# Performance work log

Hardware: AMD Instinct MI355X
Metric: run time of the kernel (lower is better)

## Reference

```python
import jax, jax.numpy as jnp
import numpy as np

B, S, D = 1, 2048, 2048      # batch, seq, hidden
E, F, K = 64, 512, 8         # experts, expert ffn dim, top_k


def setup_inputs() -> dict:
    key = jax.random.key(0)
    ks = jax.random.split(key, 7)
    hidden_states = jax.random.normal(ks[0], (B, S, D), jnp.float32)
    gate_w = jax.random.normal(ks[1], (E, D), jnp.float32) * (D ** -0.5)   # router Linear weight
    w_gate = jax.random.normal(ks[2], (E, F, D), jnp.float32) * 0.02       # expert gate_proj
    w_up   = jax.random.normal(ks[3], (E, F, D), jnp.float32) * 0.02       # expert up_proj
    w_down = jax.random.normal(ks[4], (E, D, F), jnp.float32) * 0.02       # expert down_proj
    token_mod  = jax.random.randint(ks[5], (B * S,), -1, 2).astype(jnp.int32)  # {-1,0,1}
    expert_mod = jax.random.randint(ks[6], (E,), -1, 2).astype(jnp.int32)      # {-1,0,1}
    return {"hidden_states": hidden_states, "gate_w": gate_w, "w_gate": w_gate,
            "w_up": w_up, "w_down": w_down, "token_mod": token_mod,
            "expert_mod": expert_mod}


def reference(hidden_states, gate_w, w_gate, w_up, w_down, token_mod, expert_mod):
    bs = B * S
    x = hidden_states.reshape(bs, D)
    # router gate (Linear, no bias): [bs, E]
    logits = x @ gate_w.T
    # modality pre-filtering: mismatch (tok*exp == -1) -> -inf before softmax
    mismatch = (token_mod[:, None] * expert_mod[None, :]) == -1
    logits = jnp.where(mismatch, -jnp.inf, logits)
    probs = jax.nn.softmax(logits, axis=-1)
    rw, sel = jax.lax.top_k(probs, K)                       # [bs,K]
    rw = rw / jnp.sum(rw, axis=-1, keepdims=True)           # renormalize
    # scatter into sparse routing tensor [bs, E]
    sparse = jnp.zeros((bs, E), x.dtype).at[jnp.arange(bs)[:, None], sel].set(rw)
    # expert dispatch (SwiGLU experts), weighted-sum combine
    g = jnp.einsum('td,efd->tef', x, w_gate)                # [bs,E,F]
    u = jnp.einsum('td,efd->tef', x, w_up)
    h = jax.nn.silu(g) * u
    out = jnp.einsum('te,tef,edf->td', sparse, h, w_down)   # [bs,D]
    return out.reshape(B, S, D)
```

## Files before the change

### kernel.cpp

```cpp
#include <hip/hip_runtime.h>
#include <math.h>

#define BS   2048
#define DIM  2048
#define NE   64
#define NF   512
#define TOPK 8
#define MAXT 320

typedef __attribute__((ext_vector_type(8))) short bf16x8;
typedef __attribute__((ext_vector_type(4))) float f32x4;

__device__ __forceinline__ unsigned cvt2(float lo, float hi) {
    unsigned r;
    asm("v_cvt_pk_bf16_f32 %0, %1, %2" : "=v"(r) : "v"(lo), "v"(hi));
    return r;
}
__device__ __forceinline__ unsigned short f2bf(float f) {
    return (unsigned short)(cvt2(f, 0.f) & 0xFFFF);
}

#define SWZ(r, b) (((((r) << 7) + (b)) ^ (((r) & 7) << 4)))

__global__ __launch_bounds__(256) void zero_kernel(float* __restrict__ out, int* __restrict__ count)
{
    const size_t idx = (size_t)blockIdx.x * blockDim.x + threadIdx.x;
    const size_t tot = (size_t)BS * DIM;
    for (size_t i = idx * 4; i < tot; i += (size_t)gridDim.x * blockDim.x * 4) {
        *(float4*)&out[i] = make_float4(0.f, 0.f, 0.f, 0.f);
    }
    if (idx < NE) count[idx] = 0;
}

__global__ __launch_bounds__(256) void cvt_x_kernel(const float* __restrict__ x,
                                                    unsigned short* __restrict__ xb)
{
    const int idx = blockIdx.x * 256 + threadIdx.x;
    const int tot = BS * DIM / 4;
    for (int i = idx; i < tot; i += gridDim.x * 256) {
        const float4 v = *(const float4*)&x[i * 4];
        *(uint2*)&xb[i * 4] = make_uint2(cvt2(v.x, v.y), cvt2(v.z, v.w));
    }
}

__global__ __launch_bounds__(256) void router_kernel(
    const float* __restrict__ x, const float* __restrict__ gate_w,
    const int* __restrict__ token_mod, const int* __restrict__ expert_mod,
    int* __restrict__ count, int* __restrict__ list_token, float* __restrict__ list_w)
{
    __shared__ float xs[4 * DIM];
    __shared__ float pr[4][NE];
    const int t0  = blockIdx.x * 4;
    const int tid = threadIdx.x;
    const int lane = tid & 63, wave = tid >> 6;

    float4* xs4 = (float4*)xs;
    const float4* xr = (const float4*)(x + (size_t)t0 * DIM);
    for (int i = tid; i < 4 * (DIM / 4); i += 256) xs4[i] = xr[i];
    __syncthreads();

    for (int j = 0; j < 16; ++j) {
        const int e = wave * 16 + j;
        const float4* gw = (const float4*)(gate_w + (size_t)e * DIM);
        float s0 = 0.f, s1 = 0.f, s2 = 0.f, s3 = 0.f;
        for (int i = lane; i < DIM / 4; i += 64) {
            const float4 g  = gw[i];
            const float4 v0 = xs4[0 * 512 + i];
            const float4 v1 = xs4[1 * 512 + i];
            const float4 v2 = xs4[2 * 512 + i];
            const float4 v3 = xs4[3 * 512 + i];
            s0 += v0.x * g.x + v0.y * g.y + v0.z * g.z + v0.w * g.w;
            s1 += v1.x * g.x + v1.y * g.y + v1.z * g.z + v1.w * g.w;
            s2 += v2.x * g.x + v2.y * g.y + v2.z * g.z + v2.w * g.w;
            s3 += v3.x * g.x + v3.y * g.y + v3.z * g.z + v3.w * g.w;
        }
        #pragma unroll
        for (int off = 32; off > 0; off >>= 1) {
            s0 += __shfl_xor(s0, off, 64);
            s1 += __shfl_xor(s1, off, 64);
            s2 += __shfl_xor(s2, off, 64);
            s3 += __shfl_xor(s3, off, 64);
        }
        if (lane == 0) {
            pr[0][e] = s0; pr[1][e] = s1; pr[2][e] = s2; pr[3][e] = s3;
        }
    }
    __syncthreads();

    {
        const int t  = t0 + wave;
        const int tm = token_mod[t];
        const int em = expert_mod[lane];
        float p = pr[wave][lane];
        if (tm * em == -1) p = -INFINITY;
        float m0 = p;
        #pragma unroll
        for (int off = 32; off > 0; off >>= 1) m0 = fmaxf(m0, __shfl_xor(m0, off, 64));
        p = __expf(p - m0);
        float s8 = 0.f, wsel = 0.f;
        int   esel = 0;
        #pragma unroll
        for (int k = 0; k < TOPK; ++k) {
            float m = p;
            #pragma unroll
            for (int off = 32; off > 0; off >>= 1) m = fmaxf(m, __shfl_xor(m, off, 64));
            const unsigned long long b = __ballot(p == m);
            const int bi = __ffsll((unsigned long long)b) - 1;
            if (lane == bi) p = -1.f;
            if (lane == k) { esel = bi; wsel = m; }
            s8 += m;
        }
        const float inv = 1.f / s8;
        if (lane < TOPK) {
            const int pos = atomicAdd(&count[esel], 1);
            list_token[esel * BS + pos] = t;
            list_w[esel * BS + pos]     = wsel * inv;
        }
    }
}

__global__ void scan_kernel(const int* __restrict__ count, int* __restrict__ offsets,
                            int* __restrict__ worklist, int* __restrict__ ntiles)
{
    if (threadIdx.x == 0) {
        int s = 0, nt = 0;
        for (int e = 0; e < NE; ++e) {
            offsets[e] = s;
            for (int m0 = 0; m0 < count[e]; m0 += 64) worklist[nt++] = (e << 16) | m0;
            s += count[e];
        }
        ntiles[0] = nt;
    }
}

#define GU_X   0
#define GU_G   8192
#define GU_U   16384

#define GU_COMPUTE()                                                                  \
    {                                                                                 \
        _Pragma("unroll")                                                             \
        for (int ks = 0; ks < 2; ++ks) {                                              \
            const int kb = (ks * 32 + (lane >> 4) * 8) * 2;                           \
            bf16x8 a[2], bg[2], bu[2];                                                \
            _Pragma("unroll")                                                         \
            for (int m = 0; m < 2; ++m)                                               \
                a[m] = *(const bf16x8*)&lds[GU_X + SWZ(wr * 32 + m * 16 + (lane & 15), kb)]; \
            _Pragma("unroll")                                                         \
            for (int nn = 0; nn < 2; ++nn) {                                          \
                const int r = wc * 32 + nn * 16 + (lane & 15);                        \
                bg[nn] = *(const bf16x8*)&lds[GU_G + SWZ(r, kb)];                     \
                bu[nn] = *(const bf16x8*)&lds[GU_U + SWZ(r, kb)];                     \
            }                                                                         \
            _Pragma("unroll")                                                         \
            for (int m = 0; m < 2; ++m)                                               \
                _Pragma("unroll")                                                     \
                for (int nn = 0; nn < 2; ++nn) {                                      \
                    accg[m][nn] = __builtin_amdgcn_mfma_f32_16x16x32_bf16(a[m], bg[nn], accg[m][nn], 0, 0, 0); \
                    accu[m][nn] = __builtin_amdgcn_mfma_f32_16x16x32_bf16(a[m], bu[nn], accu[m][nn], 0, 0, 0); \
                }                                                                     \
        }                                                                             \
    }

#define GU_WRITE()                                                                    \
    {                                                                                 \
        _Pragma("unroll")                                                             \
        for (int i = 0; i < 2; ++i)                                                   \
            *(uint4*)&lds[GU_X + SWZ(xr0 + i * 32, xb0 * 16)] = lxx[i];               \
        _Pragma("unroll")                                                             \
        for (int i = 0; i < 4; ++i) {                                                 \
            const int r = rr + i * 16;                                                \
            *(uint2*)&lds[GU_G + SWZ(r, c4 * 8)] = make_uint2(cvt2(lg[i].x, lg[i].y), cvt2(lg[i].z, lg[i].w)); \
            *(uint2*)&lds[GU_U + SWZ(r, c4 * 8)] = make_uint2(cvt2(lu[i].x, lu[i].y), cvt2(lu[i].z, lu[i].w)); \
        }                                                                             \
    }

__global__ __launch_bounds__(256, 3) void gateup_mfma(
    const unsigned short* __restrict__ xb,
    const float* __restrict__ w_gate, const float* __restrict__ w_up,
    const int* __restrict__ count, const int* __restrict__ offsets,
    const int* __restrict__ worklist, const int* __restrict__ ntiles,
    const int* __restrict__ list_token, const float* __restrict__ list_w,
    unsigned short* __restrict__ h)
{
    if ((int)blockIdx.y >= ntiles[0]) return;
    const int wl = worklist[blockIdx.y];
    const int e  = wl >> 16;
    const int m0 = wl & 0xFFFF;
    const int f0 = blockIdx.x * 64;
    const int mc = min(64, count[e] - m0);

    __shared__ char  lds[24576];
    __shared__ int   toks[64];
    __shared__ float rws[64];

    const int tid = threadIdx.x;
    if (tid < 64) {
        const int idx = e * BS + m0 + (tid < mc ? tid : 0);
        toks[tid] = list_token[idx];
        rws[tid]  = (tid < mc) ? list_w[idx] : 0.f;
    }
    __syncthreads();

    const int lane = tid & 63, wave = tid >> 6;
    const int wr = wave >> 1, wc = wave & 1;
    const int rr = tid >> 4;
    const int c4 = tid & 15;
    const int xr0 = tid >> 3;
    const int xb0 = tid & 7;

    const unsigned short* xrow[2];
    #pragma unroll
    for (int i = 0; i < 2; ++i)
        xrow[i] = xb + (size_t)toks[xr0 + i * 32] * DIM + xb0 * 8;
    const float* grow[4];
    const float* urow[4];
    #pragma unroll
    for (int i = 0; i < 4; ++i) {
        grow[i] = w_gate + (size_t)e * NF * DIM + (size_t)(f0 + rr + i * 16) * DIM + c4 * 4;
        urow[i] = w_up   + (size_t)e * NF * DIM + (size_t)(f0 + rr + i * 16) * DIM + c4 * 4;
    }

    f32x4 accg[2][2] = {};
    f32x4 accu[2][2] = {};
    uint4  lxx[2];
    float4 lg[4], lu[4];

    #pragma unroll
    for (int i = 0; i < 2; ++i) lxx[i] = *(const uint4*)(xrow[i]);
    #pragma unroll
    for (int i = 0; i < 4; ++i) {
        lg[i] = *(const float4*)(grow[i]);
        lu[i] = *(const float4*)(urow[i]);
    }
    GU_WRITE();
    __syncthreads();

    for (int t = 0; t < DIM / 64 - 1; ++t) {
        const int doff = (t + 1) * 64;
        #pragma unroll
        for (int i = 0; i < 2; ++i) lxx[i] = *(const uint4*)(xrow[i] + doff);
        #pragma unroll
        for (int i = 0; i < 4; ++i) {
            lg[i] = *(const float4*)(grow[i] + doff);
            lu[i] = *(const float4*)(urow[i] + doff);
        }
        __builtin_amdgcn_sched_barrier(0);
        GU_COMPUTE();
        __syncthreads();
        GU_WRITE();
        __syncthreads();
    }
    GU_COMPUTE();

    const int base = offsets[e] + m0;
    #pragma unroll
    for (int m = 0; m < 2; ++m) {
        #pragma unroll
        for (int j = 0; j < 4; ++j) {
            const int tl = wr * 32 + m * 16 + (lane >> 4) * 4 + j;
            if (tl < mc) {
                const float w = rws[tl];
                #pragma unroll
                for (int nn = 0; nn < 2; ++nn) {
                    const int fl = f0 + wc * 32 + nn * 16 + (lane & 15);
                    const float g  = accg[m][nn][j];
                    const float u  = accu[m][nn][j];
                    const float hv = w * u * (g / (1.f + __expf(-g)));
                    h[(size_t)(base + tl) * NF + fl] = f2bf(hv);
                }
            }
        }
    }
}

#define DK_H   0
#define DK_W   8192

#define DK_COMPUTE()                                                                  \
    {                                                                                 \
        _Pragma("unroll")                                                             \
        for (int ks = 0; ks < 2; ++ks) {                                              \
            const int kb = (ks * 32 + (lane >> 4) * 8) * 2;                           \
            bf16x8 a[2], b[4];                                                        \
            _Pragma("unroll")                                                         \
            for (int m = 0; m < 2; ++m)                                               \
                a[m] = *(const bf16x8*)&lds[DK_H + SWZ(wr * 32 + m * 16 + (lane & 15), kb)]; \
            _Pragma("unroll")                                                         \
            for (int nn = 0; nn < 4; ++nn)                                            \
                b[nn] = *(const bf16x8*)&lds[DK_W + SWZ(wc * 64 + nn * 16 + (lane & 15), kb)]; \
            _Pragma("unroll")                                                         \
            for (int m = 0; m < 2; ++m)                                               \
                _Pragma("unroll")                                                     \
                for (int nn = 0; nn < 4; ++nn)                                        \
                    acc[m][nn] = __builtin_amdgcn_mfma_f32_16x16x32_bf16(a[m], b[nn], acc[m][nn], 0, 0, 0); \
        }                                                                             \
    }

#define DK_WRITE()                                                                    \
    {                                                                                 \
        _Pragma("unroll")                                                             \
        for (int i = 0; i < 2; ++i)                                                   \
            *(uint4*)&lds[DK_H + SWZ(hr + i * 32, hc * 2)] = lh[i];                   \
        _Pragma("unroll")                                                             \
        for (int i = 0; i < 8; ++i)                                                   \
            *(uint2*)&lds[DK_W + SWZ(rr + i * 16, c4 * 8)] = make_uint2(cvt2(lw[i].x, lw[i].y), cvt2(lw[i].z, lw[i].w)); \
    }

__global__ __launch_bounds__(256, 3) void down_mfma(
    const float* __restrict__ w_down,
    const int* __restrict__ count, const int* __restrict__ offsets,
    const int* __restrict__ worklist, const int* __restrict__ ntiles,
    const int* __restrict__ list_token,
    const unsigned short* __restrict__ h, float* __restrict__ out)
{
    if ((int)blockIdx.y >= ntiles[0]) return;
    const int wl = worklist[blockIdx.y];
    const int e  = wl >> 16;
    const int m0 = wl & 0xFFFF;
    const int d0 = blockIdx.x * 128;
    const int mc = min(64, count[e] - m0);

    __shared__ char lds[24576];
    __shared__ int  toks[64];

    const int tid = threadIdx.x;
    if (tid < 64) toks[tid] = list_token[e * BS + m0 + (tid < mc ? tid : 0)];
    __syncthreads();

    const int lane = tid & 63, wave = tid >> 6;
    const int wr = wave >> 1, wc = wave & 1;
    const int rr = tid >> 4;
    const int c4 = tid & 15;
    const int hr = tid >> 3;
    const int hc = (tid & 7) * 8;

    const float* wd  = w_down + (size_t)e * DIM * NF;
    const int   base = offsets[e] + m0;

    const unsigned short* hrow[2];
    #pragma unroll
    for (int i = 0; i < 2; ++i) {
        const int r  = hr + i * 32;
        const int rs = (r < mc ? r : 0);
        hrow[i] = h + (size_t)(base + rs) * NF + hc;
    }
    const float* wrow[8];
    #pragma unroll
    for (int i = 0; i < 8; ++i) wrow[i] = wd + (size_t)(d0 + rr + i * 16) * NF + c4 * 4;

    f32x4 acc[2][4] = {};
    uint4  lh[2];
    float4 lw[8];

    #pragma unroll
    for (int i = 0; i < 2; ++i) lh[i] = *(const uint4*)(hrow[i]);
    #pragma unroll
    for (int i = 0; i < 8; ++i) lw[i] = *(const float4*)(wrow[i]);
    DK_WRITE();
    __syncthreads();

    for (int t = 0; t < NF / 64 - 1; ++t) {
        const int foff = (t + 1) * 64;
        #pragma unroll
        for (int i = 0; i < 2; ++i) lh[i] = *(const uint4*)(hrow[i] + foff);
        #pragma unroll
        for (int i = 0; i < 8; ++i) lw[i] = *(const float4*)(wrow[i] + foff);
        __builtin_amdgcn_sched_barrier(0);
        DK_COMPUTE();
        __syncthreads();
        DK_WRITE();
        __syncthreads();
    }
    DK_COMPUTE();

    #pragma unroll
    for (int m = 0; m < 2; ++m)
        #pragma unroll
        for (int j = 0; j < 4; ++j) {
            const int sl = wr * 32 + m * 16 + (lane >> 4) * 4 + j;
            if (sl < mc) {
                float* orow = out + (size_t)toks[sl] * DIM + d0 + wc * 64 + (lane & 15);
                #pragma unroll
                for (int nn = 0; nn < 4; ++nn)
                    atomicAdd(&orow[nn * 16], acc[m][nn][j]);
            }
        }
}

extern "C" void kernel_launch(void* const* d_in, const int* in_sizes, int n_in,
                              void* d_out, int out_size, void* d_ws, size_t ws_size,
                              hipStream_t stream)
{
    const float* x          = (const float*)d_in[0];
    const float* gate_w     = (const float*)d_in[1];
    const float* w_gate     = (const float*)d_in[2];
    const float* w_up       = (const float*)d_in[3];
    const float* w_down     = (const float*)d_in[4];
    const int*   token_mod  = (const int*)d_in[5];
    const int*   expert_mod = (const int*)d_in[6];
    float* out = (float*)d_out;

    char* ws = (char*)d_ws;
    unsigned short* h  = (unsigned short*)ws;
    unsigned short* xb = (unsigned short*)(ws + 16777216);
    int*   count      = (int*)(ws + 25165824);
    int*   offsets    = (int*)(ws + 25166080);
    int*   ntiles     = (int*)(ws + 25166336);
    int*   worklist   = (int*)(ws + 25166592);
    int*   list_token = (int*)(ws + 25168640);
    float* list_w     = (float*)(ws + 25692928);

    zero_kernel<<<2048, 256, 0, stream>>>(out, count);
    cvt_x_kernel<<<1024, 256, 0, stream>>>(x, xb);
    router_kernel<<<BS / 4, 256, 0, stream>>>(x, gate_w, token_mod, expert_mod,
                                              count, list_token, list_w);
    scan_kernel<<<1, 64, 0, stream>>>(count, offsets, worklist, ntiles);

    dim3 g1(NF / 64, MAXT);
    gateup_mfma<<<g1, 256, 0, stream>>>(xb, w_gate, w_up, count, offsets,
                                        worklist, ntiles, list_token, list_w, h);
    dim3 g2(DIM / 128, MAXT);
    down_mfma<<<g2, 256, 0, stream>>>(w_down, count, offsets, worklist, ntiles,
                                      list_token, h, out);
}
```

Before: 625.9 us.

## Drop LDS staging; load MFMA operands directly from global with register double-buffering

Both expert GEMM kernels stop staging x/h and weight tiles through shared memory. Each lane now loads its MFMA fragments straight from global memory, converting weights to bf16 in registers, and double-buffers the loads across k-steps with no barriers. This removes the LDS round trip and the __syncthreads pairs. The cost is that weight rows are no longer shared between the waves in a block, so there are more global loads and more register pressure, and the occupancy bound is lowered from 3 to 2.

```diff
diff --git a/kernel.cpp b/kernel.cpp
--- a/kernel.cpp
+++ b/kernel.cpp
@@ -19,8 +19,12 @@
 __device__ __forceinline__ unsigned short f2bf(float f) {
     return (unsigned short)(cvt2(f, 0.f) & 0xFFFF);
 }
-
-#define SWZ(r, b) (((((r) << 7) + (b)) ^ (((r) & 7) << 4)))
+__device__ __forceinline__ bf16x8 pk8(float4 lo, float4 hi) {
+    union { bf16x8 v; unsigned u[4]; } r;
+    r.u[0] = cvt2(lo.x, lo.y); r.u[1] = cvt2(lo.z, lo.w);
+    r.u[2] = cvt2(hi.x, hi.y); r.u[3] = cvt2(hi.z, hi.w);
+    return r.v;
+}
 
 __global__ __launch_bounds__(256) void zero_kernel(float* __restrict__ out, int* __restrict__ count)
 {
@@ -133,49 +137,40 @@
     }
 }
 
-#define GU_X   0
-#define GU_G   8192
-#define GU_U   16384
-
-#define GU_COMPUTE()                                                                  \
-    {                                                                                 \
-        _Pragma("unroll")                                                             \
-        for (int ks = 0; ks < 2; ++ks) {                                              \
-            const int kb = (ks * 32 + (lane >> 4) * 8) * 2;                           \
-            bf16x8 a[2], bg[2], bu[2];                                                \
-            _Pragma("unroll")                                                         \
-            for (int m = 0; m < 2; ++m)                                               \
-                a[m] = *(const bf16x8*)&lds[GU_X + SWZ(wr * 32 + m * 16 + (lane & 15), kb)]; \
-            _Pragma("unroll")                                                         \
-            for (int nn = 0; nn < 2; ++nn) {                                          \
-                const int r = wc * 32 + nn * 16 + (lane & 15);                        \
-                bg[nn] = *(const bf16x8*)&lds[GU_G + SWZ(r, kb)];                     \
-                bu[nn] = *(const bf16x8*)&lds[GU_U + SWZ(r, kb)];                     \
-            }                                                                         \
-            _Pragma("unroll")                                                         \
-            for (int m = 0; m < 2; ++m)                                               \
-                _Pragma("unroll")                                                     \
-                for (int nn = 0; nn < 2; ++nn) {                                      \
-                    accg[m][nn] = __builtin_amdgcn_mfma_f32_16x16x32_bf16(a[m], bg[nn], accg[m][nn], 0, 0, 0); \
-                    accu[m][nn] = __builtin_amdgcn_mfma_f32_16x16x32_bf16(a[m], bu[nn], accu[m][nn], 0, 0, 0); \
-                }                                                                     \
-        }                                                                             \
-    }
-
-#define GU_WRITE()                                                                    \
-    {                                                                                 \
-        _Pragma("unroll")                                                             \
-        for (int i = 0; i < 2; ++i)                                                   \
-            *(uint4*)&lds[GU_X + SWZ(xr0 + i * 32, xb0 * 16)] = lxx[i];               \
-        _Pragma("unroll")                                                             \
-        for (int i = 0; i < 4; ++i) {                                                 \
-            const int r = rr + i * 16;                                                \
-            *(uint2*)&lds[GU_G + SWZ(r, c4 * 8)] = make_uint2(cvt2(lg[i].x, lg[i].y), cvt2(lg[i].z, lg[i].w)); \
-            *(uint2*)&lds[GU_U + SWZ(r, c4 * 8)] = make_uint2(cvt2(lu[i].x, lu[i].y), cvt2(lu[i].z, lu[i].w)); \
-        }                                                                             \
-    }
-
-__global__ __launch_bounds__(256, 3) void gateup_mfma(
+struct B8 { float4 v[8]; };
+
+
+#define GU_LOADB(BUF, KO)                                                     \
+    {                                                                         \
+        _Pragma("unroll")                                                     \
+        for (int nn = 0; nn < 2; ++nn) {                                      \
+            (BUF).v[nn * 2 + 0] = *(const float4*)(gp[nn] + (KO));            \
+            (BUF).v[nn * 2 + 1] = *(const float4*)(gp[nn] + (KO) + 4);        \
+            (BUF).v[4 + nn * 2 + 0] = *(const float4*)(up[nn] + (KO));        \
+            (BUF).v[4 + nn * 2 + 1] = *(const float4*)(up[nn] + (KO) + 4);    \
+        }                                                                     \
+    }
+
+#define GU_STEP(BUF, KO)                                                      \
+    {                                                                         \
+        bf16x8 a[2], bg[2], bu[2];                                            \
+        _Pragma("unroll")                                                     \
+        for (int m = 0; m < 2; ++m) a[m] = *(const bf16x8*)(aptr[m] + (KO));  \
+        _Pragma("unroll")                                                     \
+        for (int nn = 0; nn < 2; ++nn) {                                      \
+            bg[nn] = pk8((BUF).v[nn * 2], (BUF).v[nn * 2 + 1]);               \
+            bu[nn] = pk8((BUF).v[4 + nn * 2], (BUF).v[4 + nn * 2 + 1]);       \
+        }                                                                     \
+        _Pragma("unroll")                                                     \
+        for (int m = 0; m < 2; ++m)                                           \
+            _Pragma("unroll")                                                 \
+            for (int nn = 0; nn < 2; ++nn) {                                  \
+                accg[m][nn] = __builtin_amdgcn_mfma_f32_16x16x32_bf16(a[m], bg[nn], accg[m][nn], 0, 0, 0); \
+                accu[m][nn] = __builtin_amdgcn_mfma_f32_16x16x32_bf16(a[m], bu[nn], accu[m][nn], 0, 0, 0); \
+            }                                                                 \
+    }
+
+__global__ __launch_bounds__(256, 2) void gateup_mfma(
     const unsigned short* __restrict__ xb,
     const float* __restrict__ w_gate, const float* __restrict__ w_up,
     const int* __restrict__ count, const int* __restrict__ offsets,
@@ -190,68 +185,38 @@
     const int f0 = blockIdx.x * 64;
     const int mc = min(64, count[e] - m0);
 
-    __shared__ char  lds[24576];
-    __shared__ int   toks[64];
-    __shared__ float rws[64];
-
     const int tid = threadIdx.x;
-    if (tid < 64) {
-        const int idx = e * BS + m0 + (tid < mc ? tid : 0);
-        toks[tid] = list_token[idx];
-        rws[tid]  = (tid < mc) ? list_w[idx] : 0.f;
-    }
-    __syncthreads();
-
     const int lane = tid & 63, wave = tid >> 6;
     const int wr = wave >> 1, wc = wave & 1;
-    const int rr = tid >> 4;
-    const int c4 = tid & 15;
-    const int xr0 = tid >> 3;
-    const int xb0 = tid & 7;
-
-    const unsigned short* xrow[2];
-    #pragma unroll
-    for (int i = 0; i < 2; ++i)
-        xrow[i] = xb + (size_t)toks[xr0 + i * 32] * DIM + xb0 * 8;
-    const float* grow[4];
-    const float* urow[4];
-    #pragma unroll
-    for (int i = 0; i < 4; ++i) {
-        grow[i] = w_gate + (size_t)e * NF * DIM + (size_t)(f0 + rr + i * 16) * DIM + c4 * 4;
-        urow[i] = w_up   + (size_t)e * NF * DIM + (size_t)(f0 + rr + i * 16) * DIM + c4 * 4;
+    const int kq = (lane >> 4) * 8;
+
+    const unsigned short* aptr[2];
+    #pragma unroll
+    for (int m = 0; m < 2; ++m) {
+        const int r = wr * 32 + m * 16 + (lane & 15);
+        const int t = list_token[e * BS + m0 + (r < mc ? r : 0)];
+        aptr[m] = xb + (size_t)t * DIM + kq;
+    }
+    const float* gp[2];
+    const float* up[2];
+    #pragma unroll
+    for (int nn = 0; nn < 2; ++nn) {
+        const int fr = f0 + wc * 32 + nn * 16 + (lane & 15);
+        gp[nn] = w_gate + (size_t)e * NF * DIM + (size_t)fr * DIM + kq;
+        up[nn] = w_up   + (size_t)e * NF * DIM + (size_t)fr * DIM + kq;
     }
 
     f32x4 accg[2][2] = {};
     f32x4 accu[2][2] = {};
-    uint4  lxx[2];
-    float4 lg[4], lu[4];
-
-    #pragma unroll
-    for (int i = 0; i < 2; ++i) lxx[i] = *(const uint4*)(xrow[i]);
-    #pragma unroll
-    for (int i = 0; i < 4; ++i) {
-        lg[i] = *(const float4*)(grow[i]);
-        lu[i] = *(const float4*)(urow[i]);
-    }
-    GU_WRITE();
-    __syncthreads();
-
-    for (int t = 0; t < DIM / 64 - 1; ++t) {
-        const int doff = (t + 1) * 64;
-        #pragma unroll
-        for (int i = 0; i < 2; ++i) lxx[i] = *(const uint4*)(xrow[i] + doff);
-        #pragma unroll
-        for (int i = 0; i < 4; ++i) {
-            lg[i] = *(const float4*)(grow[i] + doff);
-            lu[i] = *(const float4*)(urow[i] + doff);
-        }
-        __builtin_amdgcn_sched_barrier(0);
-        GU_COMPUTE();
-        __syncthreads();
-        GU_WRITE();
-        __syncthreads();
-    }
-    GU_COMPUTE();
+    B8 bufA, bufB;
+
+    GU_LOADB(bufA, 0);
+    for (int t = 0; t < DIM / 32; t += 2) {
+        GU_LOADB(bufB, (t + 1) * 32);
+        GU_STEP(bufA, t * 32);
+        if (t + 2 < DIM / 32) GU_LOADB(bufA, (t + 2) * 32);
+        GU_STEP(bufB, (t + 1) * 32);
+    }
 
     const int base = offsets[e] + m0;
     #pragma unroll
@@ -260,7 +225,7 @@
         for (int j = 0; j < 4; ++j) {
             const int tl = wr * 32 + m * 16 + (lane >> 4) * 4 + j;
             if (tl < mc) {
-                const float w = rws[tl];
+                const float w = list_w[e * BS + m0 + tl];
                 #pragma unroll
                 for (int nn = 0; nn < 2; ++nn) {
                     const int fl = f0 + wc * 32 + nn * 16 + (lane & 15);
@@ -274,40 +239,32 @@
     }
 }
 
-#define DK_H   0
-#define DK_W   8192
-
-#define DK_COMPUTE()                                                                  \
-    {                                                                                 \
-        _Pragma("unroll")                                                             \
-        for (int ks = 0; ks < 2; ++ks) {                                              \
-            const int kb = (ks * 32 + (lane >> 4) * 8) * 2;                           \
-            bf16x8 a[2], b[4];                                                        \
-            _Pragma("unroll")                                                         \
-            for (int m = 0; m < 2; ++m)                                               \
-                a[m] = *(const bf16x8*)&lds[DK_H + SWZ(wr * 32 + m * 16 + (lane & 15), kb)]; \
-            _Pragma("unroll")                                                         \
-            for (int nn = 0; nn < 4; ++nn)                                            \
-                b[nn] = *(const bf16x8*)&lds[DK_W + SWZ(wc * 64 + nn * 16 + (lane & 15), kb)]; \
-            _Pragma("unroll")                                                         \
-            for (int m = 0; m < 2; ++m)                                               \
-                _Pragma("unroll")                                                     \
-                for (int nn = 0; nn < 4; ++nn)                                        \
-                    acc[m][nn] = __builtin_amdgcn_mfma_f32_16x16x32_bf16(a[m], b[nn], acc[m][nn], 0, 0, 0); \
-        }                                                                             \
-    }
-
-#define DK_WRITE()                                                                    \
-    {                                                                                 \
-        _Pragma("unroll")                                                             \
-        for (int i = 0; i < 2; ++i)                                                   \
-            *(uint4*)&lds[DK_H + SWZ(hr + i * 32, hc * 2)] = lh[i];                   \
-        _Pragma("unroll")                                                             \
-        for (int i = 0; i < 8; ++i)                                                   \
-            *(uint2*)&lds[DK_W + SWZ(rr + i * 16, c4 * 8)] = make_uint2(cvt2(lw[i].x, lw[i].y), cvt2(lw[i].z, lw[i].w)); \
-    }
-
-__global__ __launch_bounds__(256, 3) void down_mfma(
+
+#define DK_LOADB(BUF, KO)                                                     \
+    {                                                                         \
+        _Pragma("unroll")                                                     \
+        for (int nn = 0; nn < 4; ++nn) {                                      \
+            (BUF).v[nn * 2 + 0] = *(const float4*)(bp[nn] + (KO));            \
+            (BUF).v[nn * 2 + 1] = *(const float4*)(bp[nn] + (KO) + 4);        \
+        }                                                                     \
+    }
+
+#define DK_STEP(BUF, KO)                                                      \
+    {                                                                         \
+        bf16x8 a[2], b[4];                                                    \
+        _Pragma("unroll")                                                     \
+        for (int m = 0; m < 2; ++m) a[m] = *(const bf16x8*)(aptr[m] + (KO));  \
+        _Pragma("unroll")                                                     \
+        for (int nn = 0; nn < 4; ++nn)                                        \
+            b[nn] = pk8((BUF).v[nn * 2], (BUF).v[nn * 2 + 1]);                \
+        _Pragma("unroll")                                                     \
+        for (int m = 0; m < 2; ++m)                                           \
+            _Pragma("unroll")                                                 \
+            for (int nn = 0; nn < 4; ++nn)                                    \
+                acc[m][nn] = __builtin_amdgcn_mfma_f32_16x16x32_bf16(a[m], b[nn], acc[m][nn], 0, 0, 0); \
+    }
+
+__global__ __launch_bounds__(256, 2) void down_mfma(
     const float* __restrict__ w_down,
     const int* __restrict__ count, const int* __restrict__ offsets,
     const int* __restrict__ worklist, const int* __restrict__ ntiles,
@@ -321,58 +278,35 @@
     const int d0 = blockIdx.x * 128;
     const int mc = min(64, count[e] - m0);
 
-    __shared__ char lds[24576];
-    __shared__ int  toks[64];
-
     const int tid = threadIdx.x;
-    if (tid < 64) toks[tid] = list_token[e * BS + m0 + (tid < mc ? tid : 0)];
-    __syncthreads();
-
     const int lane = tid & 63, wave = tid >> 6;
     const int wr = wave >> 1, wc = wave & 1;
-    const int rr = tid >> 4;
-    const int c4 = tid & 15;
-    const int hr = tid >> 3;
-    const int hc = (tid & 7) * 8;
-
-    const float* wd  = w_down + (size_t)e * DIM * NF;
-    const int   base = offsets[e] + m0;
-
-    const unsigned short* hrow[2];
-    #pragma unroll
-    for (int i = 0; i < 2; ++i) {
-        const int r  = hr + i * 32;
-        const int rs = (r < mc ? r : 0);
-        hrow[i] = h + (size_t)(base + rs) * NF + hc;
-    }
-    const float* wrow[8];
-    #pragma unroll
-    for (int i = 0; i < 8; ++i) wrow[i] = wd + (size_t)(d0 + rr + i * 16) * NF + c4 * 4;
+    const int kq = (lane >> 4) * 8;
+    const int base = offsets[e] + m0;
+
+    const unsigned short* aptr[2];
+    #pragma unroll
+    for (int m = 0; m < 2; ++m) {
+        const int r = wr * 32 + m * 16 + (lane & 15);
+        aptr[m] = h + (size_t)(base + (r < mc ? r : 0)) * NF + kq;
+    }
+    const float* bp[4];
+    #pragma unroll
+    for (int nn = 0; nn < 4; ++nn) {
+        const int dr = d0 + wc * 64 + nn * 16 + (lane & 15);
+        bp[nn] = w_down + (size_t)e * DIM * NF + (size_t)dr * NF + kq;
+    }
 
     f32x4 acc[2][4] = {};
-    uint4  lh[2];
-    float4 lw[8];
-
-    #pragma unroll
-    for (int i = 0; i < 2; ++i) lh[i] = *(const uint4*)(hrow[i]);
-    #pragma unroll
-    for (int i = 0; i < 8; ++i) lw[i] = *(const float4*)(wrow[i]);
-    DK_WRITE();
-    __syncthreads();
-
-    for (int t = 0; t < NF / 64 - 1; ++t) {
-        const int foff = (t + 1) * 64;
-        #pragma unroll
-        for (int i = 0; i < 2; ++i) lh[i] = *(const uint4*)(hrow[i] + foff);
-        #pragma unroll
-        for (int i = 0; i < 8; ++i) lw[i] = *(const float4*)(wrow[i] + foff);
-        __builtin_amdgcn_sched_barrier(0);
-        DK_COMPUTE();
-        __syncthreads();
-        DK_WRITE();
-        __syncthreads();
-    }
-    DK_COMPUTE();
+    B8 bufA, bufB;
+
+    DK_LOADB(bufA, 0);
+    for (int t = 0; t < NF / 32; t += 2) {
+        DK_LOADB(bufB, (t + 1) * 32);
+        DK_STEP(bufA, t * 32);
+        if (t + 2 < NF / 32) DK_LOADB(bufA, (t + 2) * 32);
+        DK_STEP(bufB, (t + 1) * 32);
+    }
 
     #pragma unroll
     for (int m = 0; m < 2; ++m)
@@ -380,7 +314,8 @@
         for (int j = 0; j < 4; ++j) {
             const int sl = wr * 32 + m * 16 + (lane >> 4) * 4 + j;
             if (sl < mc) {
-                float* orow = out + (size_t)toks[sl] * DIM + d0 + wc * 64 + (lane & 15);
+                const int tok = list_token[e * BS + m0 + sl];
+                float* orow = out + (size_t)tok * DIM + d0 + wc * 64 + (lane & 15);
                 #pragma unroll
                 for (int nn = 0; nn < 4; ++nn)
                     atomicAdd(&orow[nn * 16], acc[m][nn][j]);
```

Measured after the change: 1.141 ms. 82.3% more time.

## Double-buffer global prefetch and swap MFMA operands for vectorized epilogue stores

Applied to the files above, without the earlier changes.

Both expert GEMM kernels now prefetch two K-stages of global loads into alternating register sets, so global latency has a full compute step to hide behind. Each stage uses one raw s_barrier plus an explicit lgkmcnt wait instead of two __syncthreads. The MFMA operands are swapped so that weights feed A and tokens feed B. Each lane then holds four consecutive F/D outputs for one token, which lets the gate-up epilogue write packed bf16 pairs as uint2 and gives the down-projection atomics contiguous addresses. The cost is more live registers for the second prefetch buffer under a 3-blocks-per-SM launch bound, which risks spills or lower occupancy.

```diff
diff --git a/kernel.cpp b/kernel.cpp
--- a/kernel.cpp
+++ b/kernel.cpp
@@ -136,44 +136,61 @@
 #define GU_X   0
 #define GU_G   8192
 #define GU_U   16384
-
-#define GU_COMPUTE()                                                                  \
-    {                                                                                 \
-        _Pragma("unroll")                                                             \
-        for (int ks = 0; ks < 2; ++ks) {                                              \
-            const int kb = (ks * 32 + (lane >> 4) * 8) * 2;                           \
-            bf16x8 a[2], bg[2], bu[2];                                                \
-            _Pragma("unroll")                                                         \
-            for (int m = 0; m < 2; ++m)                                               \
-                a[m] = *(const bf16x8*)&lds[GU_X + SWZ(wr * 32 + m * 16 + (lane & 15), kb)]; \
-            _Pragma("unroll")                                                         \
-            for (int nn = 0; nn < 2; ++nn) {                                          \
-                const int r = wc * 32 + nn * 16 + (lane & 15);                        \
-                bg[nn] = *(const bf16x8*)&lds[GU_G + SWZ(r, kb)];                     \
-                bu[nn] = *(const bf16x8*)&lds[GU_U + SWZ(r, kb)];                     \
-            }                                                                         \
-            _Pragma("unroll")                                                         \
-            for (int m = 0; m < 2; ++m)                                               \
-                _Pragma("unroll")                                                     \
-                for (int nn = 0; nn < 2; ++nn) {                                      \
-                    accg[m][nn] = __builtin_amdgcn_mfma_f32_16x16x32_bf16(a[m], bg[nn], accg[m][nn], 0, 0, 0); \
-                    accu[m][nn] = __builtin_amdgcn_mfma_f32_16x16x32_bf16(a[m], bu[nn], accu[m][nn], 0, 0, 0); \
-                }                                                                     \
-        }                                                                             \
-    }
-
-#define GU_WRITE()                                                                    \
-    {                                                                                 \
-        _Pragma("unroll")                                                             \
-        for (int i = 0; i < 2; ++i)                                                   \
-            *(uint4*)&lds[GU_X + SWZ(xr0 + i * 32, xb0 * 16)] = lxx[i];               \
-        _Pragma("unroll")                                                             \
-        for (int i = 0; i < 4; ++i) {                                                 \
-            const int r = rr + i * 16;                                                \
-            *(uint2*)&lds[GU_G + SWZ(r, c4 * 8)] = make_uint2(cvt2(lg[i].x, lg[i].y), cvt2(lg[i].z, lg[i].w)); \
-            *(uint2*)&lds[GU_U + SWZ(r, c4 * 8)] = make_uint2(cvt2(lu[i].x, lu[i].y), cvt2(lu[i].z, lu[i].w)); \
-        }                                                                             \
-    }
+#define GU_NST 32
+
+#define GU_ISSUE(S, KO)                                                       \
+    {                                                                         \
+        _Pragma("unroll")                                                     \
+        for (int i = 0; i < 2; ++i) lxx##S[i] = *(const uint4*)(xrow[i] + (KO)); \
+        _Pragma("unroll")                                                     \
+        for (int i = 0; i < 4; ++i) {                                         \
+            lg##S[i] = *(const float4*)(grow[i] + (KO));                      \
+            lu##S[i] = *(const float4*)(urow[i] + (KO));                      \
+        }                                                                     \
+    }
+
+#define GU_LDSW(S)                                                            \
+    {                                                                         \
+        _Pragma("unroll")                                                     \
+        for (int i = 0; i < 2; ++i)                                           \
+            *(uint4*)&lds[GU_X + SWZ(xr0 + i * 32, xb0 * 16)] = lxx##S[i];    \
+        _Pragma("unroll")                                                     \
+        for (int i = 0; i < 4; ++i) {                                         \
+            const int r = rr + i * 16;                                        \
+            *(uint2*)&lds[GU_G + SWZ(r, c4 * 8)] = make_uint2(cvt2(lg##S[i].x, lg##S[i].y), cvt2(lg##S[i].z, lg##S[i].w)); \
+            *(uint2*)&lds[GU_U + SWZ(r, c4 * 8)] = make_uint2(cvt2(lu##S[i].x, lu##S[i].y), cvt2(lu##S[i].z, lu##S[i].w)); \
+        }                                                                     \
+    }
+
+#define GU_COMPUTE()                                                          \
+    {                                                                         \
+        _Pragma("unroll")                                                     \
+        for (int ks = 0; ks < 2; ++ks) {                                      \
+            const int kb = (ks * 32 + (lane >> 4) * 8) * 2;                   \
+            bf16x8 bx[2], ag[2], au[2];                                       \
+            _Pragma("unroll")                                                 \
+            for (int nt = 0; nt < 2; ++nt)                                    \
+                bx[nt] = *(const bf16x8*)&lds[GU_X + SWZ(wr * 32 + nt * 16 + (lane & 15), kb)]; \
+            _Pragma("unroll")                                                 \
+            for (int mm = 0; mm < 2; ++mm) {                                  \
+                const int r = wc * 32 + mm * 16 + (lane & 15);                \
+                ag[mm] = *(const bf16x8*)&lds[GU_G + SWZ(r, kb)];             \
+                au[mm] = *(const bf16x8*)&lds[GU_U + SWZ(r, kb)];             \
+            }                                                                 \
+            _Pragma("unroll")                                                 \
+            for (int mm = 0; mm < 2; ++mm)                                    \
+                _Pragma("unroll")                                             \
+                for (int nt = 0; nt < 2; ++nt) {                              \
+                    accg[mm][nt] = __builtin_amdgcn_mfma_f32_16x16x32_bf16(ag[mm], bx[nt], accg[mm][nt], 0, 0, 0); \
+                    accu[mm][nt] = __builtin_amdgcn_mfma_f32_16x16x32_bf16(au[mm], bx[nt], accu[mm][nt], 0, 0, 0); \
+                }                                                             \
+        }                                                                     \
+    }
+
+#define GU_SYNC_W()                                                           \
+    asm volatile("s_waitcnt lgkmcnt(0)" ::: "memory");                        \
+    __builtin_amdgcn_sched_barrier(0);                                        \
+    __builtin_amdgcn_s_barrier();
 
 __global__ __launch_bounds__(256, 3) void gateup_mfma(
     const unsigned short* __restrict__ xb,
@@ -223,52 +240,50 @@
 
     f32x4 accg[2][2] = {};
     f32x4 accu[2][2] = {};
-    uint4  lxx[2];
-    float4 lg[4], lu[4];
-
-    #pragma unroll
-    for (int i = 0; i < 2; ++i) lxx[i] = *(const uint4*)(xrow[i]);
-    #pragma unroll
-    for (int i = 0; i < 4; ++i) {
-        lg[i] = *(const float4*)(grow[i]);
-        lu[i] = *(const float4*)(urow[i]);
-    }
-    GU_WRITE();
-    __syncthreads();
-
-    for (int t = 0; t < DIM / 64 - 1; ++t) {
-        const int doff = (t + 1) * 64;
+    uint4  lxxE[2], lxxO[2];
+    float4 lgE[4], luE[4], lgO[4], luO[4];
+
+    GU_ISSUE(E, 0);
+    GU_ISSUE(O, 64);
+    __builtin_amdgcn_sched_barrier(0);
+    GU_LDSW(E);
+    GU_SYNC_W();
+
+    for (int t = 0; t < GU_NST; t += 2) {
+        if (t + 2 < GU_NST) { GU_ISSUE(E, (t + 2) * 64); __builtin_amdgcn_sched_barrier(0); }
+        GU_COMPUTE();
+        __builtin_amdgcn_sched_barrier(0);
+        __builtin_amdgcn_s_barrier();
+        GU_LDSW(O);
+        GU_SYNC_W();
+        if (t + 3 < GU_NST) { GU_ISSUE(O, (t + 3) * 64); __builtin_amdgcn_sched_barrier(0); }
+        GU_COMPUTE();
+        if (t + 2 < GU_NST) {
+            __builtin_amdgcn_sched_barrier(0);
+            __builtin_amdgcn_s_barrier();
+            GU_LDSW(E);
+            GU_SYNC_W();
+        }
+    }
+
+    const int base = offsets[e] + m0;
+    #pragma unroll
+    for (int mm = 0; mm < 2; ++mm) {
         #pragma unroll
-        for (int i = 0; i < 2; ++i) lxx[i] = *(const uint4*)(xrow[i] + doff);
-        #pragma unroll
-        for (int i = 0; i < 4; ++i) {
-            lg[i] = *(const float4*)(grow[i] + doff);
-            lu[i] = *(const float4*)(urow[i] + doff);
-        }
-        __builtin_amdgcn_sched_barrier(0);
-        GU_COMPUTE();
-        __syncthreads();
-        GU_WRITE();
-        __syncthreads();
-    }
-    GU_COMPUTE();
-
-    const int base = offsets[e] + m0;
-    #pragma unroll
-    for (int m = 0; m < 2; ++m) {
-        #pragma unroll
-        for (int j = 0; j < 4; ++j) {
-            const int tl = wr * 32 + m * 16 + (lane >> 4) * 4 + j;
+        for (int nt = 0; nt < 2; ++nt) {
+            const int tl = wr * 32 + nt * 16 + (lane & 15);
             if (tl < mc) {
                 const float w = rws[tl];
+                float hv[4];
                 #pragma unroll
-                for (int nn = 0; nn < 2; ++nn) {
-                    const int fl = f0 + wc * 32 + nn * 16 + (lane & 15);
-                    const float g  = accg[m][nn][j];
-                    const float u  = accu[m][nn][j];
-                    const float hv = w * u * (g / (1.f + __expf(-g)));
-                    h[(size_t)(base + tl) * NF + fl] = f2bf(hv);
+                for (int j = 0; j < 4; ++j) {
+                    const float g = accg[mm][nt][j];
+                    const float u = accu[mm][nt][j];
+                    hv[j] = w * u * (g / (1.f + __expf(-g)));
                 }
+                const int fl = f0 + wc * 32 + mm * 16 + (lane >> 4) * 4;
+                *(uint2*)&h[(size_t)(base + tl) * NF + fl] =
+                    make_uint2(cvt2(hv[0], hv[1]), cvt2(hv[2], hv[3]));
             }
         }
     }
@@ -276,35 +291,44 @@
 
 #define DK_H   0
 #define DK_W   8192
-
-#define DK_COMPUTE()                                                                  \
-    {                                                                                 \
-        _Pragma("unroll")                                                             \
-        for (int ks = 0; ks < 2; ++ks) {                                              \
-            const int kb = (ks * 32 + (lane >> 4) * 8) * 2;                           \
-            bf16x8 a[2], b[4];                                                        \
-            _Pragma("unroll")                                                         \
-            for (int m = 0; m < 2; ++m)                                               \
-                a[m] = *(const bf16x8*)&lds[DK_H + SWZ(wr * 32 + m * 16 + (lane & 15), kb)]; \
-            _Pragma("unroll")                                                         \
-            for (int nn = 0; nn < 4; ++nn)                                            \
-                b[nn] = *(const bf16x8*)&lds[DK_W + SWZ(wc * 64 + nn * 16 + (lane & 15), kb)]; \
-            _Pragma("unroll")                                                         \
-            for (int m = 0; m < 2; ++m)                                               \
-                _Pragma("unroll")                                                     \
-                for (int nn = 0; nn < 4; ++nn)                                        \
-                    acc[m][nn] = __builtin_amdgcn_mfma_f32_16x16x32_bf16(a[m], b[nn], acc[m][nn], 0, 0, 0); \
-        }                                                                             \
-    }
-
-#define DK_WRITE()                                                                    \
-    {                                                                                 \
-        _Pragma("unroll")                                                             \
-        for (int i = 0; i < 2; ++i)                                                   \
-            *(uint4*)&lds[DK_H + SWZ(hr + i * 32, hc * 2)] = lh[i];                   \
-        _Pragma("unroll")                                                             \
-        for (int i = 0; i < 8; ++i)                                                   \
-            *(uint2*)&lds[DK_W + SWZ(rr + i * 16, c4 * 8)] = make_uint2(cvt2(lw[i].x, lw[i].y), cvt2(lw[i].z, lw[i].w)); \
+#define DK_NST 8
+
+#define DK_ISSUE(S, KO)                                                       \
+    {                                                                         \
+        _Pragma("unroll")                                                     \
+        for (int i = 0; i < 2; ++i) lh##S[i] = *(const uint4*)(hrow[i] + (KO)); \
+        _Pragma("unroll")                                                     \
+        for (int i = 0; i < 8; ++i) lw##S[i] = *(const float4*)(wrow[i] + (KO)); \
+    }
+
+#define DK_LDSW(S)                                                            \
+    {                                                                         \
+        _Pragma("unroll")                                                     \
+        for (int i = 0; i < 2; ++i)                                           \
+            *(uint4*)&lds[DK_H + SWZ(hr + i * 32, hc * 2)] = lh##S[i];        \
+        _Pragma("unroll")                                                     \
+        for (int i = 0; i < 8; ++i)                                           \
+            *(uint2*)&lds[DK_W + SWZ(rr + i * 16, c4 * 8)] = make_uint2(cvt2(lw##S[i].x, lw##S[i].y), cvt2(lw##S[i].z, lw##S[i].w)); \
+    }
+
+#define DK_COMPUTE()                                                          \
+    {                                                                         \
+        _Pragma("unroll")                                                     \
+        for (int ks = 0; ks < 2; ++ks) {                                      \
+            const int kb = (ks * 32 + (lane >> 4) * 8) * 2;                   \
+            bf16x8 bh[2], aw[4];                                              \
+            _Pragma("unroll")                                                 \
+            for (int nt = 0; nt < 2; ++nt)                                    \
+                bh[nt] = *(const bf16x8*)&lds[DK_H + SWZ(wr * 32 + nt * 16 + (lane & 15), kb)]; \
+            _Pragma("unroll")                                                 \
+            for (int dd = 0; dd < 4; ++dd)                                    \
+                aw[dd] = *(const bf16x8*)&lds[DK_W + SWZ(wc * 64 + dd * 16 + (lane & 15), kb)]; \
+            _Pragma("unroll")                                                 \
+            for (int dd = 0; dd < 4; ++dd)                                    \
+                _Pragma("unroll")                                             \
+                for (int nt = 0; nt < 2; ++nt)                                \
+                    acc[dd][nt] = __builtin_amdgcn_mfma_f32_16x16x32_bf16(aw[dd], bh[nt], acc[dd][nt], 0, 0, 0); \
+        }                                                                     \
     }
 
 __global__ __launch_bounds__(256, 3) void down_mfma(
@@ -349,41 +373,44 @@
     #pragma unroll
     for (int i = 0; i < 8; ++i) wrow[i] = wd + (size_t)(d0 + rr + i * 16) * NF + c4 * 4;
 
-    f32x4 acc[2][4] = {};
-    uint4  lh[2];
-    float4 lw[8];
-
-    #pragma unroll
-    for (int i = 0; i < 2; ++i) lh[i] = *(const uint4*)(hrow[i]);
-    #pragma unroll
-    for (int i = 0; i < 8; ++i) lw[i] = *(const float4*)(wrow[i]);
-    DK_WRITE();
-    __syncthreads();
-
-    for (int t = 0; t < NF / 64 - 1; ++t) {
-        const int foff = (t + 1) * 64;
+    f32x4 acc[4][2] = {};
+    uint4  lhE[2], lhO[2];
+    float4 lwE[8], lwO[8];
+
+    DK_ISSUE(E, 0);
+    DK_ISSUE(O, 64);
+    __builtin_amdgcn_sched_barrier(0);
+    DK_LDSW(E);
+    GU_SYNC_W();
+
+    for (int t = 0; t < DK_NST; t += 2) {
+        if (t + 2 < DK_NST) { DK_ISSUE(E, (t + 2) * 64); __builtin_amdgcn_sched_barrier(0); }
+        DK_COMPUTE();
+        __builtin_amdgcn_sched_barrier(0);
+        __builtin_amdgcn_s_barrier();
+        DK_LDSW(O);
+        GU_SYNC_W();
+        if (t + 3 < DK_NST) { DK_ISSUE(O, (t + 3) * 64); __builtin_amdgcn_sched_barrier(0); }
+        DK_COMPUTE();
+        if (t + 2 < DK_NST) {
+            __builtin_amdgcn_sched_barrier(0);
+            __builtin_amdgcn_s_barrier();
+            DK_LDSW(E);
+            GU_SYNC_W();
+        }
+    }
+
+    #pragma unroll
+    for (int dd = 0; dd < 4; ++dd)
         #pragma unroll
-        for (int i = 0; i < 2; ++i) lh[i] = *(const uint4*)(hrow[i] + foff);
-        #pragma unroll
-        for (int i = 0; i < 8; ++i) lw[i] = *(const float4*)(wrow[i] + foff);
-        __builtin_amdgcn_sched_barrier(0);
-        DK_COMPUTE();
-        __syncthreads();
-        DK_WRITE();
-        __syncthreads();
-    }
-    DK_COMPUTE();
-
-    #pragma unroll
-    for (int m = 0; m < 2; ++m)
-        #pragma unroll
-        for (int j = 0; j < 4; ++j) {
-            const int sl = wr * 32 + m * 16 + (lane >> 4) * 4 + j;
-            if (sl < mc) {
-                float* orow = out + (size_t)toks[sl] * DIM + d0 + wc * 64 + (lane & 15);
+        for (int nt = 0; nt < 2; ++nt) {
+            const int tl = wr * 32 + nt * 16 + (lane & 15);
+            if (tl < mc) {
+                const int tok = toks[tl];
+                float* orow = out + (size_t)tok * DIM + d0 + wc * 64 + dd * 16 + (lane >> 4) * 4;
                 #pragma unroll
-                for (int nn = 0; nn < 4; ++nn)
-                    atomicAdd(&orow[nn * 16], acc[m][nn][j]);
+                for (int j = 0; j < 4; ++j)
+                    atomicAdd(&orow[j], acc[dd][nt][j]);
             }
         }
 }
```

New measurement: 1.361 ms. +117.5%, slower.
